# Kernel optimization log

Hardware: AMD Instinct MI355X
Metric: run time of the kernel (lower is better)

Reference implementation:

```python
import jax, jax.numpy as jnp
import numpy as np

T, H, P = 8192, 512, 512
DT_MIN, DT_MAX = 0.001, 0.1
STEP_RESCALE = 1.0


def setup_inputs() -> dict:
    key = jax.random.key(0)
    ks = jax.random.split(key, 8)
    x = jax.random.normal(ks[0], (T, H), dtype=jnp.float32)
    # sparse reset flags (episode boundaries)
    mask = jax.random.bernoulli(ks[1], 0.005, (T,)).astype(jnp.float32)
    carry = jnp.zeros((1, P, 2), dtype=jnp.float32)  # initial complex state as (re, im)
    # HiPPO-DPLR-style eigenvalue init: lambda_k = -0.5 + i*pi*k
    lambda_real = -0.5 * jnp.ones((P,), dtype=jnp.float32)
    lambda_imag = jnp.pi * jnp.arange(P, dtype=jnp.float32)
    b = jax.random.normal(ks[2], (P, H, 2), dtype=jnp.float32) / np.sqrt(H)
    c = jax.random.normal(ks[3], (H, P, 2), dtype=jnp.float32) * np.sqrt(0.5)
    d = jax.random.normal(ks[4], (H,), dtype=jnp.float32)
    u = jax.random.uniform(ks[5], (P, 1), dtype=jnp.float32)
    log_step = np.log(DT_MIN) + u * (np.log(DT_MAX) - np.log(DT_MIN))
    return {"x": x, "mask": mask, "carry": carry, "lambda_real": lambda_real,
            "lambda_imag": lambda_imag, "b": b, "c": c, "d": d, "log_step": log_step}


def _binary_operator_reset(q_i, q_j):
    a_i, b_i, c_i = q_i
    a_j, b_j, c_j = q_j
    a_out = a_j * a_i * (1.0 - c_j) + a_j * c_j
    b_out = (a_j * b_i + b_j) * (1.0 - c_j) + b_j * c_j
    c_out = c_i * (1.0 - c_j) + c_j
    return (a_out, b_out, c_out)


def reference(x, mask, carry, lambda_real, lambda_imag, b, c, d, log_step):
    t = x.shape[0]
    # clip_eigens=True: force stability
    lam_re = jnp.minimum(lambda_real, -0.0001)
    lam = jax.lax.complex(lam_re, lambda_imag).astype(jnp.complex64)  # [P]
    b_tilde = jax.lax.complex(b[..., 0], b[..., 1]).astype(jnp.complex64)  # [P,H]
    c_tilde = jax.lax.complex(c[..., 0], c[..., 1]).astype(jnp.complex64)  # [H,P]
    step = (STEP_RESCALE * jnp.exp(log_step[:, 0].astype(jnp.float32))).astype(jnp.complex64)  # [P]
    # ZOH discretization
    lambda_bar = jnp.exp(lam * step)                      # [P]
    b_bar = ((lambda_bar - 1.0) / lam)[:, None] * b_tilde  # [P,H]
    # scan elements
    a = jnp.broadcast_to(lambda_bar, (t, P))
    a = jnp.concatenate([jnp.ones((1, P), dtype=lambda_bar.dtype), a])  # [T+1,P]
    b_x = x.astype(jnp.complex64) @ b_bar.T                              # [T,P]
    carry0 = jax.lax.complex(carry[..., 0], carry[..., 1]).astype(jnp.complex64)  # [1,P]
    b_x = jnp.concatenate([carry0, b_x])                                 # [T+1,P]
    m = jnp.concatenate([jnp.zeros((1,), x.dtype), mask])[:, None]       # [T+1,1]
    _, states, _ = jax.lax.associative_scan(_binary_operator_reset, (a, b_x, m))
    states = states[1:]                                                  # [T,P] complex
    ys = jnp.real(states @ c_tilde.T) + d * x                            # [T,H]
    final_carry = states[-1][None]                                       # [1,P] complex
    return (final_carry, ys)
```

## Files before the change

kernel.cpp:

```cpp
#include <hip/hip_runtime.h>
#include <hip/hip_bf16.h>

#define T_LEN 8192
#define H_DIM 512
#define P_DIM 512
#define CS 32
#define NB (T_LEN / CS)

typedef __attribute__((ext_vector_type(8))) __bf16 bf16x8;
typedef __attribute__((ext_vector_type(4))) float f32x4;

__device__ __forceinline__ unsigned short f2bf(float f) {
    __bf16 h = (__bf16)f;
    return __builtin_bit_cast(unsigned short, h);
}
__device__ __forceinline__ float bf2f(unsigned short u) {
    unsigned v = ((unsigned)u) << 16;
    return __builtin_bit_cast(float, v);
}

__device__ __forceinline__ void gload_lds16(void* g, void* l) {
    __builtin_amdgcn_global_load_lds(
        (__attribute__((address_space(1))) unsigned*)g,
        (__attribute__((address_space(3))) unsigned*)l, 16, 0, 0);
}

__global__ __launch_bounds__(512) void precompute_p1(
    const float* __restrict__ lambda_real,
    const float* __restrict__ lambda_imag,
    const float* __restrict__ log_step,
    double* __restrict__ lbar,
    double* __restrict__ coef) {
    int p = threadIdx.x;
    double lr = fmin((double)lambda_real[p], -1e-4);
    double li = (double)lambda_imag[p];
    double step = exp((double)log_step[p]);
    double er = exp(lr * step);
    double ang = li * step;
    double lbr = er * cos(ang);
    double lbi = er * sin(ang);
    lbar[2 * p] = lbr;
    lbar[2 * p + 1] = lbi;
    double nr = lbr - 1.0, ni = lbi;
    double den = lr * lr + li * li;
    coef[2 * p]     = (nr * lr + ni * li) / den;
    coef[2 * p + 1] = (ni * lr - nr * li) / den;
}

__global__ __launch_bounds__(256) void conv_x_kernel(
    const float* __restrict__ x,
    unsigned short* __restrict__ xhi, unsigned short* __restrict__ xlo) {
    int idx = blockIdx.x * 256 + threadIdx.x;
    float2 v = ((const float2*)x)[idx];
    ushort2 h, l;
    h.x = f2bf(v.x); l.x = f2bf(v.x - bf2f(h.x));
    h.y = f2bf(v.y); l.y = f2bf(v.y - bf2f(h.y));
    ((ushort2*)xhi)[idx] = h;
    ((ushort2*)xlo)[idx] = l;
}

__global__ __launch_bounds__(256) void fillB_kernel(
    const float* __restrict__ b, const float* __restrict__ c,
    const double* __restrict__ coef,
    unsigned short* __restrict__ Bt1hi, unsigned short* __restrict__ Bt1lo,
    unsigned short* __restrict__ Bt2hi, unsigned short* __restrict__ Bt2lo) {
    int idx = blockIdx.x * 256 + threadIdx.x;
    {
        int p = idx >> 9, h = idx & 511;
        double cr = coef[2 * p], ci = coef[2 * p + 1];
        float2 bv = ((const float2*)b)[(size_t)p * H_DIM + h];
        float re = (float)(cr * (double)bv.x - ci * (double)bv.y);
        float im = (float)(cr * (double)bv.y + ci * (double)bv.x);
        unsigned short rh = f2bf(re), ih = f2bf(im);
        Bt1hi[(size_t)(2 * p) * H_DIM + h]     = rh;
        Bt1lo[(size_t)(2 * p) * H_DIM + h]     = f2bf(re - bf2f(rh));
        Bt1hi[(size_t)(2 * p + 1) * H_DIM + h] = ih;
        Bt1lo[(size_t)(2 * p + 1) * H_DIM + h] = f2bf(im - bf2f(ih));
    }
    {
        int h = idx >> 9, p = idx & 511;
        float2 cv = ((const float2*)c)[(size_t)h * P_DIM + p];
        float re = cv.x, im = -cv.y;
        ushort2 hi, lo;
        hi.x = f2bf(re); lo.x = f2bf(re - bf2f(hi.x));
        hi.y = f2bf(im); lo.y = f2bf(im - bf2f(hi.y));
        ((ushort2*)Bt2hi)[(size_t)h * P_DIM + p] = hi;
        ((ushort2*)Bt2lo)[(size_t)h * P_DIM + p] = lo;
    }
}

template <int MODE>
__global__ __launch_bounds__(256) void gemm_mfma_split(
    const unsigned short* __restrict__ Ahi, const unsigned short* __restrict__ Alo,
    int lda,
    const unsigned short* __restrict__ Bthi, const unsigned short* __restrict__ Btlo,
    int ldb,
    void* __restrict__ Cout0, void* __restrict__ Cout1, int ldc, int K,
    const float* __restrict__ Dvec, const float* __restrict__ X) {
    __shared__ __align__(16) unsigned short lds[2][4][128 * 32];
    const int tid = threadIdx.x;
    const int lane = tid & 63, wid = tid >> 6;
    const int wm = wid >> 1, wn = wid & 1;
    const int bm = blockIdx.y * 128, bn = blockIdx.x * 128;

    const unsigned short* ssrc;
    int srow0, sld;
    if (wid == 0)      { ssrc = Ahi;  srow0 = bm; sld = lda; }
    else if (wid == 1) { ssrc = Alo;  srow0 = bm; sld = lda; }
    else if (wid == 2) { ssrc = Bthi; srow0 = bn; sld = ldb; }
    else               { ssrc = Btlo; srow0 = bn; sld = ldb; }

    f32x4 acc[4][4];
#pragma unroll
    for (int i = 0; i < 4; ++i)
#pragma unroll
        for (int j = 0; j < 4; ++j) acc[i][j] = (f32x4)(0.0f);

    auto stage = [&](int buf, int k0) {
        unsigned short* base = &lds[buf][wid][0];
#pragma unroll
        for (int s = 0; s < 8; ++s) {
            int r = s * 16 + (lane >> 2);
            int cg = (lane & 3) ^ ((r >> 1) & 3);
            void* g = (void*)((const char*)(ssrc + (size_t)(srow0 + r) * sld + k0)
                              + cg * 16);
            gload_lds16(g, (void*)((char*)base + s * 1024));
        }
    };

    stage(0, 0);
    __syncthreads();

    const int nk = K / 32;
    for (int t = 0; t < nk; ++t) {
        int cur = t & 1;
        if (t + 1 < nk) stage(cur ^ 1, (t + 1) * 32);

        bf16x8 ah[4], al[4], bh[4], bl[4];
#pragma unroll
        for (int i = 0; i < 4; ++i) {
            int rA = wm * 64 + i * 16 + (lane & 15);
            int byA = rA * 64 + ((((lane >> 4)) ^ ((rA >> 1) & 3)) << 4);
            ah[i] = *(const bf16x8*)((const char*)&lds[cur][0][0] + byA);
            al[i] = *(const bf16x8*)((const char*)&lds[cur][1][0] + byA);
            int rB = wn * 64 + i * 16 + (lane & 15);
            int byB = rB * 64 + ((((lane >> 4)) ^ ((rB >> 1) & 3)) << 4);
            bh[i] = *(const bf16x8*)((const char*)&lds[cur][2][0] + byB);
            bl[i] = *(const bf16x8*)((const char*)&lds[cur][3][0] + byB);
        }
#pragma unroll
        for (int i = 0; i < 4; ++i)
#pragma unroll
            for (int j = 0; j < 4; ++j) {
                acc[i][j] = __builtin_amdgcn_mfma_f32_16x16x32_bf16(
                    ah[i], bh[j], acc[i][j], 0, 0, 0);
                acc[i][j] = __builtin_amdgcn_mfma_f32_16x16x32_bf16(
                    ah[i], bl[j], acc[i][j], 0, 0, 0);
                acc[i][j] = __builtin_amdgcn_mfma_f32_16x16x32_bf16(
                    al[i], bh[j], acc[i][j], 0, 0, 0);
            }
        __syncthreads();
    }

#pragma unroll
    for (int i = 0; i < 4; ++i)
#pragma unroll
        for (int j = 0; j < 4; ++j) {
            int col = bn + wn * 64 + j * 16 + (lane & 15);
#pragma unroll
            for (int r = 0; r < 4; ++r) {
                int row = bm + wm * 64 + i * 16 + (lane >> 4) * 4 + r;
                float v = acc[i][j][r];
                if (MODE == 0) {
                    unsigned short h = f2bf(v);
                    unsigned short lo = f2bf(v - bf2f(h));
                    ((unsigned short*)Cout0)[(size_t)row * ldc + col] = h;
                    ((unsigned short*)Cout1)[(size_t)row * ldc + col] = lo;
                } else {
                    v += Dvec[col] * X[(size_t)row * ldc + col];
                    ((float*)Cout0)[(size_t)row * ldc + col] = v;
                }
            }
        }
}

__global__ __launch_bounds__(512) void scanA_kernel(
    const unsigned short* __restrict__ Shi, const unsigned short* __restrict__ Slo,
    const float* __restrict__ mask, const double* __restrict__ lbar,
    double* __restrict__ cA, double* __restrict__ cS, float* __restrict__ cC) {
    int p = threadIdx.x;
    int blk = blockIdx.x;
    double lbr = lbar[2 * p], lbi = lbar[2 * p + 1];
    double Ar = 1., Ai = 0., Sr = 0., Si = 0.;
    float C = 0.f;
    const ushort2* H2 = (const ushort2*)Shi;
    const ushort2* L2 = (const ushort2*)Slo;
    int t0 = blk * CS;
    for (int t = t0; t < t0 + CS; ++t) {
        float m = mask[t];
        ushort2 h2 = H2[(size_t)t * P_DIM + p];
        ushort2 l2 = L2[(size_t)t * P_DIM + p];
        double bxr = (double)(bf2f(h2.x) + bf2f(l2.x));
        double bxi = (double)(bf2f(h2.y) + bf2f(l2.y));
        if (m != 0.f) {
            Ar = lbr; Ai = lbi; Sr = bxr; Si = bxi; C = 1.f;
        } else {
            double nAr = lbr * Ar - lbi * Ai;
            Ai = lbr * Ai + lbi * Ar; Ar = nAr;
            double nSr = lbr * Sr - lbi * Si + bxr;
            Si = lbr * Si + lbi * Sr + bxi; Sr = nSr;
        }
    }
    cA[(size_t)blk * 1024 + 2 * p] = Ar;
    cA[(size_t)blk * 1024 + 2 * p + 1] = Ai;
    cS[(size_t)blk * 1024 + 2 * p] = Sr;
    cS[(size_t)blk * 1024 + 2 * p + 1] = Si;
    cC[(size_t)blk * P_DIM + p] = C;
}

__global__ __launch_bounds__(256) void scanB_kernel(
    const double* __restrict__ cA, const double* __restrict__ cS,
    const float* __restrict__ cC, const float* __restrict__ carry,
    double* __restrict__ prefix) {
    int p = blockIdx.x;
    int i = threadIdx.x;
    __shared__ double sAr[NB], sAi[NB], sSr[NB], sSi[NB];
    __shared__ float sC[NB];

    double Ar = cA[(size_t)i * 1024 + 2 * p];
    double Ai = cA[(size_t)i * 1024 + 2 * p + 1];
    double Sr = cS[(size_t)i * 1024 + 2 * p];
    double Si = cS[(size_t)i * 1024 + 2 * p + 1];
    float  C  = cC[(size_t)i * P_DIM + p];
    sAr[i] = Ar; sAi[i] = Ai; sSr[i] = Sr; sSi[i] = Si; sC[i] = C;
    __syncthreads();

    for (int step = 1; step < NB; step <<= 1) {
        double pAr = 0, pAi = 0, pSr = 0, pSi = 0; float pC = 0;
        if (i >= step) {
            pAr = sAr[i - step]; pAi = sAi[i - step];
            pSr = sSr[i - step]; pSi = sSi[i - step]; pC = sC[i - step];
        }
        __syncthreads();
        if (i >= step && C == 0.f) {
            double nAr = Ar * pAr - Ai * pAi;
            double nAi = Ar * pAi + Ai * pAr;
            double nSr = Ar * pSr - Ai * pSi + Sr;
            double nSi = Ar * pSi + Ai * pSr + Si;
            Ar = nAr; Ai = nAi; Sr = nSr; Si = nSi; C = pC;
        }
        sAr[i] = Ar; sAi[i] = Ai; sSr[i] = Sr; sSi[i] = Si; sC[i] = C;
        __syncthreads();
    }

    double c0r = (double)carry[2 * p], c0i = (double)carry[2 * p + 1];
    double pr, pi_;
    if (i == 0) {
        pr = c0r; pi_ = c0i;
    } else {
        double Lr = sAr[i - 1], Li = sAi[i - 1];
        double Tr = sSr[i - 1], Ti = sSi[i - 1];
        float  LC = sC[i - 1];
        if (LC != 0.f) { pr = Tr; pi_ = Ti; }
        else {
            pr  = Lr * c0r - Li * c0i + Tr;
            pi_ = Lr * c0i + Li * c0r + Ti;
        }
    }
    prefix[(size_t)i * 1024 + 2 * p]     = pr;
    prefix[(size_t)i * 1024 + 2 * p + 1] = pi_;
}

__global__ __launch_bounds__(512) void scanC_kernel(
    unsigned short* __restrict__ Shi, unsigned short* __restrict__ Slo,
    const float* __restrict__ mask, const double* __restrict__ lbar,
    const double* __restrict__ prefix,
    float* __restrict__ carry_out, int carry_elems) {
    int p = threadIdx.x;
    int blk = blockIdx.x;
    double lbr = lbar[2 * p], lbi = lbar[2 * p + 1];
    double sr = prefix[(size_t)blk * 1024 + 2 * p];
    double si = prefix[(size_t)blk * 1024 + 2 * p + 1];
    ushort2* H2 = (ushort2*)Shi;
    ushort2* L2 = (ushort2*)Slo;
    int t0 = blk * CS;
    for (int t = t0; t < t0 + CS; ++t) {
        float m = mask[t];
        ushort2 h2 = H2[(size_t)t * P_DIM + p];
        ushort2 l2 = L2[(size_t)t * P_DIM + p];
        double bxr = (double)(bf2f(h2.x) + bf2f(l2.x));
        double bxi = (double)(bf2f(h2.y) + bf2f(l2.y));
        if (m != 0.f) {
            sr = bxr; si = bxi;
        } else {
            double nr = lbr * sr - lbi * si + bxr;
            si = lbr * si + lbi * sr + bxi;
            sr = nr;
        }
        float sf = (float)sr, sif = (float)si;
        ushort2 ho, lo;
        ho.x = f2bf(sf);  lo.x = f2bf(sf - bf2f(ho.x));
        ho.y = f2bf(sif); lo.y = f2bf(sif - bf2f(ho.y));
        H2[(size_t)t * P_DIM + p] = ho;
        L2[(size_t)t * P_DIM + p] = lo;
    }
    if (blk == NB - 1) {
        if (carry_elems >= 1024) {
            carry_out[2 * p] = (float)sr;
            carry_out[2 * p + 1] = (float)si;
        } else {
            carry_out[p] = (float)sr;
        }
    }
}

extern "C" void kernel_launch(void* const* d_in, const int* in_sizes, int n_in,
                              void* d_out, int out_size, void* d_ws, size_t ws_size,
                              hipStream_t stream) {
    const float* x           = (const float*)d_in[0];
    const float* mask        = (const float*)d_in[1];
    const float* carry       = (const float*)d_in[2];
    const float* lambda_real = (const float*)d_in[3];
    const float* lambda_imag = (const float*)d_in[4];
    const float* b           = (const float*)d_in[5];
    const float* c           = (const float*)d_in[6];
    const float* d           = (const float*)d_in[7];
    const float* log_step    = (const float*)d_in[8];

    float* out = (float*)d_out;
    char* ws = (char*)d_ws;

    int carry_elems = out_size - T_LEN * H_DIM;
    if (carry_elems != 512 && carry_elems != 1024) carry_elems = 1024;
    float* ys_out = out + carry_elems;

    double* lbar   = (double*)ws;                        ws += 1024 * 8;
    double* coef   = (double*)ws;                        ws += 1024 * 8;
    double* cA     = (double*)ws;                        ws += (size_t)NB * 1024 * 8;
    double* cSb    = (double*)ws;                        ws += (size_t)NB * 1024 * 8;
    double* prefix = (double*)ws;                        ws += (size_t)NB * 1024 * 8;
    float* cC      = (float*)ws;                         ws += (size_t)NB * P_DIM * 4;
    unsigned short* xhi   = (unsigned short*)ws;         ws += (size_t)T_LEN * H_DIM * 2;
    unsigned short* xlo   = (unsigned short*)ws;         ws += (size_t)T_LEN * H_DIM * 2;
    unsigned short* Bt1hi = (unsigned short*)ws;         ws += (size_t)(2 * P_DIM) * H_DIM * 2;
    unsigned short* Bt1lo = (unsigned short*)ws;         ws += (size_t)(2 * P_DIM) * H_DIM * 2;
    unsigned short* Bt2hi = (unsigned short*)ws;         ws += (size_t)H_DIM * (2 * P_DIM) * 2;
    unsigned short* Bt2lo = (unsigned short*)ws;         ws += (size_t)H_DIM * (2 * P_DIM) * 2;
    unsigned short* Shi   = (unsigned short*)ws;         ws += (size_t)T_LEN * (2 * P_DIM) * 2;
    unsigned short* Slo   = (unsigned short*)ws;         ws += (size_t)T_LEN * (2 * P_DIM) * 2;

    precompute_p1<<<1, 512, 0, stream>>>(lambda_real, lambda_imag, log_step,
                                         lbar, coef);
    conv_x_kernel<<<(T_LEN * H_DIM / 2) / 256, 256, 0, stream>>>(x, xhi, xlo);
    fillB_kernel<<<(P_DIM * H_DIM) / 256, 256, 0, stream>>>(b, c, coef,
                                                            Bt1hi, Bt1lo,
                                                            Bt2hi, Bt2lo);

    {
        dim3 grid((2 * P_DIM) / 128, T_LEN / 128);
        gemm_mfma_split<0><<<grid, 256, 0, stream>>>(
            xhi, xlo, H_DIM, Bt1hi, Bt1lo, H_DIM,
            Shi, Slo, 2 * P_DIM, H_DIM, nullptr, nullptr);
    }

    scanA_kernel<<<NB, 512, 0, stream>>>(Shi, Slo, mask, lbar, cA, cSb, cC);
    scanB_kernel<<<P_DIM, NB, 0, stream>>>(cA, cSb, cC, carry, prefix);
    scanC_kernel<<<NB, 512, 0, stream>>>(Shi, Slo, mask, lbar, prefix, out,
                                         carry_elems);

    {
        dim3 grid(H_DIM / 128, T_LEN / 128);
        gemm_mfma_split<1><<<grid, 256, 0, stream>>>(
            Shi, Slo, 2 * P_DIM, Bt2hi, Bt2lo, 2 * P_DIM,
            ys_out, nullptr, H_DIM, 2 * P_DIM, d, x);
    }
}
```

Baseline: 122.1 us.

## Fuse input conversion kernels and remap GEMM blocks for XCD-local L2 reuse

Merges the x conversion and B/C matrix fill kernels into a single prep kernel, removing one launch and its gap. Also remaps the GEMM block indices so that blocks dispatched round-robin to the same XCD cover a contiguous band of rows. This is meant to raise L2 reuse of the A and B tiles per chiplet. The remap assumes gridDim.y is divisible by 8.

```diff
diff --git a/kernel.cpp b/kernel.cpp
--- a/kernel.cpp
+++ b/kernel.cpp
@@ -47,45 +47,45 @@
     coef[2 * p + 1] = (ni * lr - nr * li) / den;
 }
 
-__global__ __launch_bounds__(256) void conv_x_kernel(
+__global__ __launch_bounds__(256) void prep_kernel(
     const float* __restrict__ x,
-    unsigned short* __restrict__ xhi, unsigned short* __restrict__ xlo) {
-    int idx = blockIdx.x * 256 + threadIdx.x;
-    float2 v = ((const float2*)x)[idx];
-    ushort2 h, l;
-    h.x = f2bf(v.x); l.x = f2bf(v.x - bf2f(h.x));
-    h.y = f2bf(v.y); l.y = f2bf(v.y - bf2f(h.y));
-    ((ushort2*)xhi)[idx] = h;
-    ((ushort2*)xlo)[idx] = l;
-}
-
-__global__ __launch_bounds__(256) void fillB_kernel(
     const float* __restrict__ b, const float* __restrict__ c,
     const double* __restrict__ coef,
+    unsigned short* __restrict__ xhi, unsigned short* __restrict__ xlo,
     unsigned short* __restrict__ Bt1hi, unsigned short* __restrict__ Bt1lo,
     unsigned short* __restrict__ Bt2hi, unsigned short* __restrict__ Bt2lo) {
     int idx = blockIdx.x * 256 + threadIdx.x;
     {
-        int p = idx >> 9, h = idx & 511;
-        double cr = coef[2 * p], ci = coef[2 * p + 1];
-        float2 bv = ((const float2*)b)[(size_t)p * H_DIM + h];
-        float re = (float)(cr * (double)bv.x - ci * (double)bv.y);
-        float im = (float)(cr * (double)bv.y + ci * (double)bv.x);
-        unsigned short rh = f2bf(re), ih = f2bf(im);
-        Bt1hi[(size_t)(2 * p) * H_DIM + h]     = rh;
-        Bt1lo[(size_t)(2 * p) * H_DIM + h]     = f2bf(re - bf2f(rh));
-        Bt1hi[(size_t)(2 * p + 1) * H_DIM + h] = ih;
-        Bt1lo[(size_t)(2 * p + 1) * H_DIM + h] = f2bf(im - bf2f(ih));
-    }
-    {
-        int h = idx >> 9, p = idx & 511;
-        float2 cv = ((const float2*)c)[(size_t)h * P_DIM + p];
-        float re = cv.x, im = -cv.y;
-        ushort2 hi, lo;
-        hi.x = f2bf(re); lo.x = f2bf(re - bf2f(hi.x));
-        hi.y = f2bf(im); lo.y = f2bf(im - bf2f(hi.y));
-        ((ushort2*)Bt2hi)[(size_t)h * P_DIM + p] = hi;
-        ((ushort2*)Bt2lo)[(size_t)h * P_DIM + p] = lo;
+        float2 v = ((const float2*)x)[idx];
+        ushort2 h, l;
+        h.x = f2bf(v.x); l.x = f2bf(v.x - bf2f(h.x));
+        h.y = f2bf(v.y); l.y = f2bf(v.y - bf2f(h.y));
+        ((ushort2*)xhi)[idx] = h;
+        ((ushort2*)xlo)[idx] = l;
+    }
+    if (blockIdx.x < (P_DIM * H_DIM) / 256) {
+        {
+            int p = idx >> 9, h = idx & 511;
+            double cr = coef[2 * p], ci = coef[2 * p + 1];
+            float2 bv = ((const float2*)b)[(size_t)p * H_DIM + h];
+            float re = (float)(cr * (double)bv.x - ci * (double)bv.y);
+            float im = (float)(cr * (double)bv.y + ci * (double)bv.x);
+            unsigned short rh = f2bf(re), ih = f2bf(im);
+            Bt1hi[(size_t)(2 * p) * H_DIM + h]     = rh;
+            Bt1lo[(size_t)(2 * p) * H_DIM + h]     = f2bf(re - bf2f(rh));
+            Bt1hi[(size_t)(2 * p + 1) * H_DIM + h] = ih;
+            Bt1lo[(size_t)(2 * p + 1) * H_DIM + h] = f2bf(im - bf2f(ih));
+        }
+        {
+            int h = idx >> 9, p = idx & 511;
+            float2 cv = ((const float2*)c)[(size_t)h * P_DIM + p];
+            float re = cv.x, im = -cv.y;
+            ushort2 hi, lo;
+            hi.x = f2bf(re); lo.x = f2bf(re - bf2f(hi.x));
+            hi.y = f2bf(im); lo.y = f2bf(im - bf2f(hi.y));
+            ((ushort2*)Bt2hi)[(size_t)h * P_DIM + p] = hi;
+            ((ushort2*)Bt2lo)[(size_t)h * P_DIM + p] = lo;
+        }
     }
 }
 
@@ -101,7 +101,13 @@
     const int tid = threadIdx.x;
     const int lane = tid & 63, wid = tid >> 6;
     const int wm = wid >> 1, wn = wid & 1;
-    const int bm = blockIdx.y * 128, bn = blockIdx.x * 128;
+
+    const int id = blockIdx.y * gridDim.x + blockIdx.x;
+    const int nx = gridDim.x, rpx = gridDim.y >> 3;
+    const int xcd = id & 7, j = id >> 3;
+    const int by = xcd * rpx + j / nx;
+    const int bx = j % nx;
+    const int bm = by * 128, bn = bx * 128;
 
     const unsigned short* ssrc;
     int srow0, sld;
@@ -114,7 +120,7 @@
 #pragma unroll
     for (int i = 0; i < 4; ++i)
 #pragma unroll
-        for (int j = 0; j < 4; ++j) acc[i][j] = (f32x4)(0.0f);
+        for (int j2 = 0; j2 < 4; ++j2) acc[i][j2] = (f32x4)(0.0f);
 
     auto stage = [&](int buf, int k0) {
         unsigned short* base = &lds[buf][wid][0];
@@ -151,13 +157,13 @@
 #pragma unroll
         for (int i = 0; i < 4; ++i)
 #pragma unroll
-            for (int j = 0; j < 4; ++j) {
-                acc[i][j] = __builtin_amdgcn_mfma_f32_16x16x32_bf16(
-                    ah[i], bh[j], acc[i][j], 0, 0, 0);
-                acc[i][j] = __builtin_amdgcn_mfma_f32_16x16x32_bf16(
-                    ah[i], bl[j], acc[i][j], 0, 0, 0);
-                acc[i][j] = __builtin_amdgcn_mfma_f32_16x16x32_bf16(
-                    al[i], bh[j], acc[i][j], 0, 0, 0);
+            for (int j2 = 0; j2 < 4; ++j2) {
+                acc[i][j2] = __builtin_amdgcn_mfma_f32_16x16x32_bf16(
+                    ah[i], bh[j2], acc[i][j2], 0, 0, 0);
+                acc[i][j2] = __builtin_amdgcn_mfma_f32_16x16x32_bf16(
+                    ah[i], bl[j2], acc[i][j2], 0, 0, 0);
+                acc[i][j2] = __builtin_amdgcn_mfma_f32_16x16x32_bf16(
+                    al[i], bh[j2], acc[i][j2], 0, 0, 0);
             }
         __syncthreads();
     }
@@ -165,12 +171,12 @@
 #pragma unroll
     for (int i = 0; i < 4; ++i)
 #pragma unroll
-        for (int j = 0; j < 4; ++j) {
-            int col = bn + wn * 64 + j * 16 + (lane & 15);
+        for (int j2 = 0; j2 < 4; ++j2) {
+            int col = bn + wn * 64 + j2 * 16 + (lane & 15);
 #pragma unroll
             for (int r = 0; r < 4; ++r) {
                 int row = bm + wm * 64 + i * 16 + (lane >> 4) * 4 + r;
-                float v = acc[i][j][r];
+                float v = acc[i][j2][r];
                 if (MODE == 0) {
                     unsigned short h = f2bf(v);
                     unsigned short lo = f2bf(v - bf2f(h));
@@ -351,10 +357,8 @@
 
     precompute_p1<<<1, 512, 0, stream>>>(lambda_real, lambda_imag, log_step,
                                          lbar, coef);
-    conv_x_kernel<<<(T_LEN * H_DIM / 2) / 256, 256, 0, stream>>>(x, xhi, xlo);
-    fillB_kernel<<<(P_DIM * H_DIM) / 256, 256, 0, stream>>>(b, c, coef,
-                                                            Bt1hi, Bt1lo,
-                                                            Bt2hi, Bt2lo);
+    prep_kernel<<<(T_LEN * H_DIM / 2) / 256, 256, 0, stream>>>(
+        x, b, c, coef, xhi, xlo, Bt1hi, Bt1lo, Bt2hi, Bt2lo);
 
     {
         dim3 grid((2 * P_DIM) / 128, T_LEN / 128);
```

Result: faster. 116.1 us (-4.9%).

## Shrink GEMM tile to 64x128, add XCD-aware block remap, fuse prep kernels

Applied to the files above, without the earlier changes.

The split-bf16 MFMA GEMMs now use 64x128 tiles instead of 128x128. This doubles the grid so more workgroups cover the CUs, and the staging loop is reworked to spread A/B segments across all four waves. Block indices are remapped so consecutive row-blocks land on the same XCD, aiming for better L2 reuse of the shared B operand. The x conversion and B/C fill kernels are merged into one launch to save a kernel dispatch. In exchange, each tile reuses less data and B is reloaded more often.

```diff
diff --git a/kernel.cpp b/kernel.cpp
--- a/kernel.cpp
+++ b/kernel.cpp
@@ -47,45 +47,45 @@
     coef[2 * p + 1] = (ni * lr - nr * li) / den;
 }
 
-__global__ __launch_bounds__(256) void conv_x_kernel(
+__global__ __launch_bounds__(256) void prep_kernel(
     const float* __restrict__ x,
-    unsigned short* __restrict__ xhi, unsigned short* __restrict__ xlo) {
-    int idx = blockIdx.x * 256 + threadIdx.x;
-    float2 v = ((const float2*)x)[idx];
-    ushort2 h, l;
-    h.x = f2bf(v.x); l.x = f2bf(v.x - bf2f(h.x));
-    h.y = f2bf(v.y); l.y = f2bf(v.y - bf2f(h.y));
-    ((ushort2*)xhi)[idx] = h;
-    ((ushort2*)xlo)[idx] = l;
-}
-
-__global__ __launch_bounds__(256) void fillB_kernel(
     const float* __restrict__ b, const float* __restrict__ c,
     const double* __restrict__ coef,
+    unsigned short* __restrict__ xhi, unsigned short* __restrict__ xlo,
     unsigned short* __restrict__ Bt1hi, unsigned short* __restrict__ Bt1lo,
     unsigned short* __restrict__ Bt2hi, unsigned short* __restrict__ Bt2lo) {
     int idx = blockIdx.x * 256 + threadIdx.x;
     {
-        int p = idx >> 9, h = idx & 511;
-        double cr = coef[2 * p], ci = coef[2 * p + 1];
-        float2 bv = ((const float2*)b)[(size_t)p * H_DIM + h];
-        float re = (float)(cr * (double)bv.x - ci * (double)bv.y);
-        float im = (float)(cr * (double)bv.y + ci * (double)bv.x);
-        unsigned short rh = f2bf(re), ih = f2bf(im);
-        Bt1hi[(size_t)(2 * p) * H_DIM + h]     = rh;
-        Bt1lo[(size_t)(2 * p) * H_DIM + h]     = f2bf(re - bf2f(rh));
-        Bt1hi[(size_t)(2 * p + 1) * H_DIM + h] = ih;
-        Bt1lo[(size_t)(2 * p + 1) * H_DIM + h] = f2bf(im - bf2f(ih));
-    }
-    {
-        int h = idx >> 9, p = idx & 511;
-        float2 cv = ((const float2*)c)[(size_t)h * P_DIM + p];
-        float re = cv.x, im = -cv.y;
-        ushort2 hi, lo;
-        hi.x = f2bf(re); lo.x = f2bf(re - bf2f(hi.x));
-        hi.y = f2bf(im); lo.y = f2bf(im - bf2f(hi.y));
-        ((ushort2*)Bt2hi)[(size_t)h * P_DIM + p] = hi;
-        ((ushort2*)Bt2lo)[(size_t)h * P_DIM + p] = lo;
+        float2 v = ((const float2*)x)[idx];
+        ushort2 h, l;
+        h.x = f2bf(v.x); l.x = f2bf(v.x - bf2f(h.x));
+        h.y = f2bf(v.y); l.y = f2bf(v.y - bf2f(h.y));
+        ((ushort2*)xhi)[idx] = h;
+        ((ushort2*)xlo)[idx] = l;
+    }
+    if (blockIdx.x < (P_DIM * H_DIM) / 256) {
+        {
+            int p = idx >> 9, h = idx & 511;
+            double cr = coef[2 * p], ci = coef[2 * p + 1];
+            float2 bv = ((const float2*)b)[(size_t)p * H_DIM + h];
+            float re = (float)(cr * (double)bv.x - ci * (double)bv.y);
+            float im = (float)(cr * (double)bv.y + ci * (double)bv.x);
+            unsigned short rh = f2bf(re), ih = f2bf(im);
+            Bt1hi[(size_t)(2 * p) * H_DIM + h]     = rh;
+            Bt1lo[(size_t)(2 * p) * H_DIM + h]     = f2bf(re - bf2f(rh));
+            Bt1hi[(size_t)(2 * p + 1) * H_DIM + h] = ih;
+            Bt1lo[(size_t)(2 * p + 1) * H_DIM + h] = f2bf(im - bf2f(ih));
+        }
+        {
+            int h = idx >> 9, p = idx & 511;
+            float2 cv = ((const float2*)c)[(size_t)h * P_DIM + p];
+            float re = cv.x, im = -cv.y;
+            ushort2 hi, lo;
+            hi.x = f2bf(re); lo.x = f2bf(re - bf2f(hi.x));
+            hi.y = f2bf(im); lo.y = f2bf(im - bf2f(hi.y));
+            ((ushort2*)Bt2hi)[(size_t)h * P_DIM + p] = hi;
+            ((ushort2*)Bt2lo)[(size_t)h * P_DIM + p] = lo;
+        }
     }
 }
 
@@ -97,34 +97,55 @@
     int ldb,
     void* __restrict__ Cout0, void* __restrict__ Cout1, int ldc, int K,
     const float* __restrict__ Dvec, const float* __restrict__ X) {
-    __shared__ __align__(16) unsigned short lds[2][4][128 * 32];
+    constexpr int BM = 64, BN = 128;
+    constexpr int MI = 2, NJ = 4;
+    constexpr int ASEG = BM / 16, BSEG = BN / 16;
+    constexpr int NSEG = 2 * ASEG + 2 * BSEG;
+    __shared__ __align__(16) unsigned short sA[2][2][BM * 32];
+    __shared__ __align__(16) unsigned short sB[2][2][BN * 32];
     const int tid = threadIdx.x;
     const int lane = tid & 63, wid = tid >> 6;
     const int wm = wid >> 1, wn = wid & 1;
-    const int bm = blockIdx.y * 128, bn = blockIdx.x * 128;
-
-    const unsigned short* ssrc;
-    int srow0, sld;
-    if (wid == 0)      { ssrc = Ahi;  srow0 = bm; sld = lda; }
-    else if (wid == 1) { ssrc = Alo;  srow0 = bm; sld = lda; }
-    else if (wid == 2) { ssrc = Bthi; srow0 = bn; sld = ldb; }
-    else               { ssrc = Btlo; srow0 = bn; sld = ldb; }
-
-    f32x4 acc[4][4];
-#pragma unroll
-    for (int i = 0; i < 4; ++i)
-#pragma unroll
-        for (int j = 0; j < 4; ++j) acc[i][j] = (f32x4)(0.0f);
+
+    const int id = blockIdx.y * gridDim.x + blockIdx.x;
+    const int nx = gridDim.x, rpx = gridDim.y >> 3;
+    const int xcd = id & 7, jj = id >> 3;
+    const int by = xcd * rpx + jj / nx;
+    const int bx = jj % nx;
+    const int bm = by * BM, bn = bx * BN;
+
+    f32x4 acc[MI][NJ];
+#pragma unroll
+    for (int i = 0; i < MI; ++i)
+#pragma unroll
+        for (int j = 0; j < NJ; ++j) acc[i][j] = (f32x4)(0.0f);
 
     auto stage = [&](int buf, int k0) {
-        unsigned short* base = &lds[buf][wid][0];
-#pragma unroll
-        for (int s = 0; s < 8; ++s) {
-            int r = s * 16 + (lane >> 2);
+#pragma unroll
+        for (int s0 = 0; s0 < NSEG / 4; ++s0) {
+            int s = s0 * 4 + wid;
+            const unsigned short* src;
+            unsigned short* dst;
+            int row0, ld, rg;
+            if (s < 2 * ASEG) {
+                int a = s >> 2;
+                rg = s & 3;
+                src = a ? Alo : Ahi;
+                dst = &sA[buf][a][0];
+                row0 = bm; ld = lda;
+            } else {
+                int t2 = s - 2 * ASEG;
+                int a = t2 >> 3;
+                rg = t2 & 7;
+                src = a ? Btlo : Bthi;
+                dst = &sB[buf][a][0];
+                row0 = bn; ld = ldb;
+            }
+            int r = rg * 16 + (lane >> 2);
             int cg = (lane & 3) ^ ((r >> 1) & 3);
-            void* g = (void*)((const char*)(ssrc + (size_t)(srow0 + r) * sld + k0)
+            void* g = (void*)((const char*)(src + (size_t)(row0 + r) * ld + k0)
                               + cg * 16);
-            gload_lds16(g, (void*)((char*)base + s * 1024));
+            gload_lds16(g, (void*)((char*)dst + rg * 1024));
         }
     };
 
@@ -136,22 +157,25 @@
         int cur = t & 1;
         if (t + 1 < nk) stage(cur ^ 1, (t + 1) * 32);
 
-        bf16x8 ah[4], al[4], bh[4], bl[4];
-#pragma unroll
-        for (int i = 0; i < 4; ++i) {
-            int rA = wm * 64 + i * 16 + (lane & 15);
+        bf16x8 ah[MI], al[MI], bh[NJ], bl[NJ];
+#pragma unroll
+        for (int i = 0; i < MI; ++i) {
+            int rA = wm * 32 + i * 16 + (lane & 15);
             int byA = rA * 64 + ((((lane >> 4)) ^ ((rA >> 1) & 3)) << 4);
-            ah[i] = *(const bf16x8*)((const char*)&lds[cur][0][0] + byA);
-            al[i] = *(const bf16x8*)((const char*)&lds[cur][1][0] + byA);
-            int rB = wn * 64 + i * 16 + (lane & 15);
+            ah[i] = *(const bf16x8*)((const char*)&sA[cur][0][0] + byA);
+            al[i] = *(const bf16x8*)((const char*)&sA[cur][1][0] + byA);
+        }
+#pragma unroll
+        for (int j = 0; j < NJ; ++j) {
+            int rB = wn * 64 + j * 16 + (lane & 15);
             int byB = rB * 64 + ((((lane >> 4)) ^ ((rB >> 1) & 3)) << 4);
-            bh[i] = *(const bf16x8*)((const char*)&lds[cur][2][0] + byB);
-            bl[i] = *(const bf16x8*)((const char*)&lds[cur][3][0] + byB);
-        }
-#pragma unroll
-        for (int i = 0; i < 4; ++i)
-#pragma unroll
-            for (int j = 0; j < 4; ++j) {
+            bh[j] = *(const bf16x8*)((const char*)&sB[cur][0][0] + byB);
+            bl[j] = *(const bf16x8*)((const char*)&sB[cur][1][0] + byB);
+        }
+#pragma unroll
+        for (int i = 0; i < MI; ++i)
+#pragma unroll
+            for (int j = 0; j < NJ; ++j) {
                 acc[i][j] = __builtin_amdgcn_mfma_f32_16x16x32_bf16(
                     ah[i], bh[j], acc[i][j], 0, 0, 0);
                 acc[i][j] = __builtin_amdgcn_mfma_f32_16x16x32_bf16(
@@ -163,13 +187,13 @@
     }
 
 #pragma unroll
-    for (int i = 0; i < 4; ++i)
-#pragma unroll
-        for (int j = 0; j < 4; ++j) {
+    for (int i = 0; i < MI; ++i)
+#pragma unroll
+        for (int j = 0; j < NJ; ++j) {
             int col = bn + wn * 64 + j * 16 + (lane & 15);
 #pragma unroll
             for (int r = 0; r < 4; ++r) {
-                int row = bm + wm * 64 + i * 16 + (lane >> 4) * 4 + r;
+                int row = bm + wm * 32 + i * 16 + (lane >> 4) * 4 + r;
                 float v = acc[i][j][r];
                 if (MODE == 0) {
                     unsigned short h = f2bf(v);
@@ -351,13 +375,11 @@
 
     precompute_p1<<<1, 512, 0, stream>>>(lambda_real, lambda_imag, log_step,
                                          lbar, coef);
-    conv_x_kernel<<<(T_LEN * H_DIM / 2) / 256, 256, 0, stream>>>(x, xhi, xlo);
-    fillB_kernel<<<(P_DIM * H_DIM) / 256, 256, 0, stream>>>(b, c, coef,
-                                                            Bt1hi, Bt1lo,
-                                                            Bt2hi, Bt2lo);
+    prep_kernel<<<(T_LEN * H_DIM / 2) / 256, 256, 0, stream>>>(
+        x, b, c, coef, xhi, xlo, Bt1hi, Bt1lo, Bt2hi, Bt2lo);
 
     {
-        dim3 grid((2 * P_DIM) / 128, T_LEN / 128);
+        dim3 grid((2 * P_DIM) / 128, T_LEN / 64);
         gemm_mfma_split<0><<<grid, 256, 0, stream>>>(
             xhi, xlo, H_DIM, Bt1hi, Bt1lo, H_DIM,
             Shi, Slo, 2 * P_DIM, H_DIM, nullptr, nullptr);
@@ -369,7 +391,7 @@
                                          carry_elems);
 
     {
-        dim3 grid(H_DIM / 128, T_LEN / 128);
+        dim3 grid(H_DIM / 128, T_LEN / 64);
         gemm_mfma_split<1><<<grid, 256, 0, stream>>>(
             Shi, Slo, 2 * P_DIM, Bt2hi, Bt2lo, 2 * P_DIM,
             ys_out, nullptr, H_DIM, 2 * P_DIM, d, x);
```

Result: slower. 370.7 us (+203.7%).
